# Optimization experiments

Hardware: AMD Instinct MI355X
Metric: run time of the kernel (lower is better)

## Reference

```python
import jax, jax.numpy as jnp
import numpy as np


def setup_inputs() -> dict:
    key = jax.random.key(0)
    kq, kk, kv = jax.random.split(key, 3)
    B, H, S, D = 2, 16, 2048, 128
    return {
        "q": jax.random.normal(kq, (B, H, S, D), dtype=jnp.float32),
        "k": jax.random.normal(kk, (B, H, S, D), dtype=jnp.float32),
        "v": jax.random.normal(kv, (B, H, S, D), dtype=jnp.float32),
    }


def reference(q, k, v):
    # scaled dot-product attention with causal mask (dropout in eval mode -> identity)
    d_k = k.shape[-1]
    scale = 1.0 / jnp.sqrt(jnp.asarray(d_k, dtype=q.dtype))
    # [B,H,Sq,Skv]
    attn = jnp.einsum("bhqd,bhkd->bhqk", q, k) * scale
    Sq = q.shape[-2]
    causal = jnp.triu(jnp.ones((Sq, Sq), dtype=bool), k=1)  # True above diagonal -> masked
    attn = jnp.where(causal, -jnp.inf, attn)
    attn = jax.nn.softmax(attn, axis=-1)
    return jnp.einsum("bhqk,bhkd->bhqd", attn, v)
```

## Files before the change

### kernel.cpp

```cpp
#include <hip/hip_runtime.h>

#define SQ 2048
#define DH 128
#define KVB 64
#define BHN 32
#define ELEMS ((size_t)BHN * SQ * DH)

typedef __bf16 bf16x8 __attribute__((ext_vector_type(8)));
typedef float f32x16 __attribute__((ext_vector_type(16)));

__device__ __forceinline__ f32x16 mfma32(bf16x8 a, bf16x8 b, f32x16 c){
  return __builtin_amdgcn_mfma_f32_32x32x16_bf16(a, b, c, 0, 0, 0);
}

#define EXP2 __builtin_amdgcn_exp2f

__device__ __forceinline__ unsigned short f2bf(float f){
  unsigned u = __builtin_bit_cast(unsigned, f);
  u += 0x7fffu + ((u >> 16) & 1u);
  return (unsigned short)(u >> 16);
}
__device__ __forceinline__ unsigned packbf(float a, float b){
  return (unsigned)f2bf(a) | ((unsigned)f2bf(b) << 16);
}

__device__ __forceinline__ void swap32(unsigned a, unsigned b, bool h, unsigned &x, unsigned &y){
  unsigned sb = __shfl_xor(b, 32);
  unsigned sa = __shfl_xor(a, 32);
  x = h ? sb : a;
  y = h ? b : sa;
}

__device__ __forceinline__ bf16x8 mkfrag(unsigned w0, unsigned w1, unsigned w2, unsigned w3){
  uint4 t; t.x = w0; t.y = w1; t.z = w2; t.w = w3;
  return __builtin_bit_cast(bf16x8, t);
}

__global__ __launch_bounds__(256, 4)
void convkv(const float* __restrict__ K, const float* __restrict__ V,
            unsigned short* __restrict__ Kb, unsigned short* __restrict__ Vb){
  const size_t g = (size_t)blockIdx.x * 256 + threadIdx.x;
  #pragma unroll
  for (int i = 0; i < 4; ++i){
    size_t e = (g + (size_t)i * 262144) * 8;
    float4 a = *(const float4*)(K + e);
    float4 b = *(const float4*)(K + e + 4);
    uint4 o;
    o.x = packbf(a.x, a.y); o.y = packbf(a.z, a.w);
    o.z = packbf(b.x, b.y); o.w = packbf(b.z, b.w);
    *(uint4*)(Kb + e) = o;
    a = *(const float4*)(V + e);
    b = *(const float4*)(V + e + 4);
    o.x = packbf(a.x, a.y); o.y = packbf(a.z, a.w);
    o.z = packbf(b.x, b.y); o.w = packbf(b.z, b.w);
    *(uint4*)(Vb + e) = o;
  }
}

template<bool BF16IN>
__global__ __launch_bounds__(512, 2)
void attn_fwd(const float* __restrict__ Q,
              const float* __restrict__ Kf,
              const float* __restrict__ Vf,
              const unsigned short* __restrict__ Kbg,
              const unsigned short* __restrict__ Vbg,
              float* __restrict__ O)
{
  __shared__ __align__(16) unsigned char smem[65536];
  float* SF = (float*)smem;

  const int tid  = threadIdx.x;
  const int lane = tid & 63;
  const int wid  = tid >> 6;
  const int rg   = wid & 3;
  const int par  = wid >> 2;
  const int col  = lane & 31;
  const int hi   = lane >> 5;
  const int i4   = lane & 3;
  const int d0   = (lane >> 2)*8;

  const int b   = blockIdx.x;
  const int xcd = b & 7;
  const int seq = b >> 3;
  const int bh4 = seq & 3;
  const int j   = seq >> 2;
  const int bh  = xcd + 8*bh4;

  const size_t base = (size_t)bh * SQ * DH;
  const float* Qg = Q + base;
  const float* Kg = Kf + base;
  const float* Vg = Vf + base;
  const unsigned short* Kgb = Kbg + base;
  const unsigned short* Vgb = Vbg + base;
  float* Og = O + base;

  const float SC = 0.08838834764831845f * 1.4426950408889634f;

  float4 kr[4], vr[4];
  uint4  krb[2], vrb[2];

  auto LOADT = [&](int kvb){
    if constexpr (BF16IN){
      #pragma unroll
      for (int i = 0; i < 2; ++i){
        int c = i*512 + tid, r = c >> 4, dc = c & 15;
        krb[i] = *(const uint4*)(Kgb + (size_t)(kvb + r)*DH + dc*8);
      }
      #pragma unroll
      for (int it = 0; it < 2; ++it){
        int row = wid*8 + it*4 + i4;
        vrb[it] = *(const uint4*)(Vgb + (size_t)(kvb + row)*DH + d0);
      }
    } else {
      #pragma unroll
      for (int i = 0; i < 2; ++i){
        int c = i*512 + tid, r = c >> 4, dc = c & 15;
        const float* src = Kg + (size_t)(kvb + r)*DH + dc*8;
        kr[2*i]   = *(const float4*)(src);
        kr[2*i+1] = *(const float4*)(src + 4);
      }
      #pragma unroll
      for (int it = 0; it < 2; ++it){
        int row = wid*8 + it*4 + i4;
        const float* src = Vg + (size_t)(kvb + row)*DH + d0;
        vr[2*it]   = *(const float4*)(src);
        vr[2*it+1] = *(const float4*)(src + 4);
      }
    }
  };

  auto STORET = [&](int bsel){
    const int bb = bsel * 32768;
    #pragma unroll
    for (int i = 0; i < 2; ++i){
      int c = i*512 + tid, r = c >> 4, dc = c & 15;
      uint4 kv;
      if constexpr (BF16IN){
        kv = krb[i];
      } else {
        kv.x = packbf(kr[2*i].x,   kr[2*i].y);
        kv.y = packbf(kr[2*i].z,   kr[2*i].w);
        kv.z = packbf(kr[2*i+1].x, kr[2*i+1].y);
        kv.w = packbf(kr[2*i+1].z, kr[2*i+1].w);
      }
      *(uint4*)&smem[bb + r*256 + ((dc*16) ^ ((r & 7) << 4))] = kv;
    }
    #pragma unroll
    for (int it = 0; it < 2; ++it){
      int r0 = wid*8 + it*4;
      unsigned M0, M1, M2, M3;
      if constexpr (BF16IN){
        M0 = vrb[it].x; M1 = vrb[it].y; M2 = vrb[it].z; M3 = vrb[it].w;
      } else {
        M0 = packbf(vr[2*it].x,   vr[2*it].y);
        M1 = packbf(vr[2*it].z,   vr[2*it].w);
        M2 = packbf(vr[2*it+1].x, vr[2*it+1].y);
        M3 = packbf(vr[2*it+1].z, vr[2*it+1].w);
      }
      unsigned t0=__shfl_xor(M1,1), t1=__shfl_xor(M0,1), t2=__shfl_xor(M3,1), t3=__shfl_xor(M2,1);
      bool ob1 = i4 & 1;
      unsigned N0 = ob1 ? t0 : M0;
      unsigned N1 = ob1 ? M1 : t1;
      unsigned N2 = ob1 ? t2 : M2;
      unsigned N3 = ob1 ? M3 : t3;
      unsigned u0s=__shfl_xor(N2,2), u1s=__shfl_xor(N3,2), u2s=__shfl_xor(N0,2), u3s=__shfl_xor(N1,2);
      bool ob2 = i4 & 2;
      unsigned F0 = ob2 ? u0s : N0;
      unsigned F1 = ob2 ? u1s : N1;
      unsigned F2 = ob2 ? N2 : u2s;
      unsigned F3 = ob2 ? N3 : u3s;
      int d = d0 + 2*i4;
      unsigned lo0 = (F0 & 0xffffu) | (F1 << 16);
      unsigned lo1 = (F2 & 0xffffu) | (F3 << 16);
      unsigned hi0 = (F0 >> 16) | (F1 & 0xffff0000u);
      unsigned hi1 = (F2 >> 16) | (F3 & 0xffff0000u);
      int cb = r0*2;
      int sA = ((d >> 1) & 7) << 4;
      *(uint2*)&smem[bb + 16384 + d*128     + (cb ^ sA)] = make_uint2(lo0, lo1);
      *(uint2*)&smem[bb + 16384 + (d+1)*128 + (cb ^ sA)] = make_uint2(hi0, hi1);
    }
  };

  #pragma unroll 1
  for (int ph = 0; ph < 2; ++ph){
    const int qt = ph ? j : (15 - j);
    const int nt = 2*qt + 2;
    const int Q0 = qt*128 + rg*32;
    const int qg = Q0 + col;

    bf16x8 qf[8];
    #pragma unroll
    for (int dc = 0; dc < 8; ++dc){
      const float* src = Qg + (size_t)qg*DH + dc*16 + hi*8;
      float4 f0 = *(const float4*)(src);
      float4 f1 = *(const float4*)(src + 4);
      uint4 tq;
      tq.x = packbf(f0.x, f0.y); tq.y = packbf(f0.z, f0.w);
      tq.z = packbf(f1.x, f1.y); tq.w = packbf(f1.z, f1.w);
      qf[dc] = __builtin_bit_cast(bf16x8, tq);
    }

    f32x16 o0 = {}, o1 = {}, o2 = {}, o3 = {};
    float m = -1e30f, lsum = 0.f;

    LOADT(0);
    STORET(0);
    __syncthreads();

    #pragma unroll 1
    for (int t = 0; t < nt; ++t){
      const int kvb = t * KVB;
      const int bb  = (t & 1) * 32768;
      const int myk = kvb + par*32;

      if (t + 1 < nt) LOADT(kvb + KVB);

      if (myk <= Q0 + 31){
        f32x16 s0 = {};
        const int krow = par*32 + col;
        #pragma unroll
        for (int dc = 0; dc < 8; ++dc){
          uint4 rk = *(const uint4*)&smem[bb + krow*256 + ((dc*32 + hi*16) ^ ((krow & 7) << 4))];
          s0 = mfma32(__builtin_bit_cast(bf16x8, rk), qf[dc], s0);
        }

        s0 = s0 * SC;
        if (myk + 31 > Q0){
          #pragma unroll
          for (int r = 0; r < 16; ++r){
            int kl = (r & 3) + 8*(r >> 2) + 4*hi;
            if (myk + kl > qg) s0[r] = -1e30f;
          }
        }

        float tmax = -1e30f;
        #pragma unroll
        for (int r = 0; r < 16; ++r) tmax = fmaxf(tmax, s0[r]);
        tmax = fmaxf(tmax, __shfl_xor(tmax, 32));
        if (!__all(tmax <= m + 8.0f)){
          float mnew  = fmaxf(m, tmax);
          float alpha = EXP2(m - mnew);
          m = mnew;
          lsum *= alpha;
          o0 *= alpha; o1 *= alpha; o2 *= alpha; o3 *= alpha;
        }

        float ps = 0.f;
        #pragma unroll
        for (int r = 0; r < 16; ++r){ float e = EXP2(s0[r] - m); s0[r] = e; ps += e; }
        lsum += ps;

        unsigned ua0 = packbf(s0[0],  s0[1]),  ua1 = packbf(s0[2],  s0[3]);
        unsigned ua2 = packbf(s0[4],  s0[5]),  ua3 = packbf(s0[6],  s0[7]);
        unsigned ua4 = packbf(s0[8],  s0[9]),  ua5 = packbf(s0[10], s0[11]);
        unsigned ua6 = packbf(s0[12], s0[13]), ua7 = packbf(s0[14], s0[15]);
        bool h = (bool)hi;
        unsigned w0, w1, w2, w3;
        bf16x8 pf[2];
        swap32(ua0, ua2, h, w0, w2); swap32(ua1, ua3, h, w1, w3); pf[0] = mkfrag(w0,w1,w2,w3);
        swap32(ua4, ua6, h, w0, w2); swap32(ua5, ua7, h, w1, w3); pf[1] = mkfrag(w0,w1,w2,w3);

        #pragma unroll
        for (int cc = 0; cc < 2; ++cc){
          #pragma unroll
          for (int db = 0; db < 4; ++db){
            int rowd = db*32 + col;
            uint4 rv = *(const uint4*)&smem[bb + 16384 + rowd*128 + ((par*64 + cc*32 + hi*16) ^ (((rowd >> 1) & 7) << 4))];
            f32x16& oo = (db==0)?o0:(db==1)?o1:(db==2)?o2:o3;
            oo = mfma32(__builtin_bit_cast(bf16x8, rv), pf[cc], oo);
          }
        }
      }

      if (t + 1 < nt) STORET((t + 1) & 1);
      __syncthreads();
    }

    lsum += __shfl_xor(lsum, 32);

    float a0 = 1.f, a1 = 0.f, inv = 0.f;
    #pragma unroll 1
    for (int round = 0; round < 2; ++round){
      const f32x16& pa = round ? o2 : o0;
      const f32x16& pb = round ? o3 : o1;
      if (par == 1){
        #pragma unroll
        for (int i = 0; i < 16; ++i){
          SF[rg*2048 + i*64 + lane]      = pa[i];
          SF[rg*2048 + (16+i)*64 + lane] = pb[i];
        }
        if (round == 0){
          SF[8192 + rg*64 + lane] = m;
          SF[8448 + rg*64 + lane] = lsum;
        }
      }
      __syncthreads();
      if (par == 0){
        if (round == 0){
          float m1 = SF[8192 + rg*64 + lane];
          float l1 = SF[8448 + rg*64 + lane];
          float ms = fmaxf(m, m1);
          a0 = EXP2(m - ms);
          a1 = EXP2(m1 - ms);
          float ls = lsum*a0 + l1*a1;
          inv = 1.0f / ls;
        }
        #pragma unroll
        for (int dbi = 0; dbi < 2; ++dbi){
          const f32x16& oo = round ? (dbi ? o3 : o2) : (dbi ? o1 : o0);
          const int db = round*2 + dbi;
          #pragma unroll
          for (int rg2 = 0; rg2 < 4; ++rg2){
            float4 w;
            w.x = (oo[rg2*4+0]*a0 + SF[rg*2048 + (dbi*16 + rg2*4+0)*64 + lane]*a1) * inv;
            w.y = (oo[rg2*4+1]*a0 + SF[rg*2048 + (dbi*16 + rg2*4+1)*64 + lane]*a1) * inv;
            w.z = (oo[rg2*4+2]*a0 + SF[rg*2048 + (dbi*16 + rg2*4+2)*64 + lane]*a1) * inv;
            w.w = (oo[rg2*4+3]*a0 + SF[rg*2048 + (dbi*16 + rg2*4+3)*64 + lane]*a1) * inv;
            *(float4*)(Og + (size_t)qg*DH + db*32 + rg2*8 + hi*4) = w;
          }
        }
      }
      __syncthreads();
    }
  }
}

extern "C" void kernel_launch(void* const* d_in, const int* in_sizes, int n_in,
                              void* d_out, int out_size, void* d_ws, size_t ws_size,
                              hipStream_t stream) {
  const float* q = (const float*)d_in[0];
  const float* k = (const float*)d_in[1];
  const float* v = (const float*)d_in[2];
  float* out = (float*)d_out;

  const size_t need = 2 * ELEMS * sizeof(unsigned short);
  if (ws_size >= need){
    unsigned short* kb = (unsigned short*)d_ws;
    unsigned short* vb = kb + ELEMS;
    convkv<<<1024, 256, 0, stream>>>(k, v, kb, vb);
    attn_fwd<true><<<256, 512, 0, stream>>>(q, k, v, kb, vb, out);
  } else {
    attn_fwd<false><<<256, 512, 0, stream>>>(q, k, v, nullptr, nullptr, out);
  }
}
```

Before: 96.29 us.

## Split paired causal q-tiles into separate blocks and add MFMA priority hints

Each block used to handle two query tiles in sequence (a long one and a short one, to balance causal work). Now each tile gets its own block, doubling the grid to 512 blocks, and the hardware scheduler does the balancing instead. Around the two MFMA loops, s_setprio is raised so matrix work is favoured over the other waves' loads. The trade-off is losing the guaranteed per-block balance and paying Q loading and setup per tile, in exchange for more concurrency and occupancy across CUs.

```diff
diff --git a/kernel.cpp b/kernel.cpp
--- a/kernel.cpp
+++ b/kernel.cpp
@@ -79,12 +79,16 @@
   const int i4   = lane & 3;
   const int d0   = (lane >> 2)*8;
 
-  const int b   = blockIdx.x;
-  const int xcd = b & 7;
-  const int seq = b >> 3;
-  const int bh4 = seq & 3;
-  const int j   = seq >> 2;
-  const int bh  = xcd + 8*bh4;
+  const int b    = blockIdx.x;
+  const int half = b >> 8;
+  const int bb8  = b & 255;
+  const int xcd  = bb8 & 7;
+  const int i    = bb8 >> 3;
+  const int bh4  = i & 3;
+  const int j    = i >> 2;
+  const int bh   = xcd + 8*bh4;
+  const int qt   = half ? j : (15 - j);
+  const int nt   = 2*qt + 2;
 
   const size_t base = (size_t)bh * SQ * DH;
   const float* Qg = Q + base;
@@ -102,9 +106,9 @@
   auto LOADT = [&](int kvb){
     if constexpr (BF16IN){
       #pragma unroll
-      for (int i = 0; i < 2; ++i){
-        int c = i*512 + tid, r = c >> 4, dc = c & 15;
-        krb[i] = *(const uint4*)(Kgb + (size_t)(kvb + r)*DH + dc*8);
+      for (int i2 = 0; i2 < 2; ++i2){
+        int c = i2*512 + tid, r = c >> 4, dc = c & 15;
+        krb[i2] = *(const uint4*)(Kgb + (size_t)(kvb + r)*DH + dc*8);
       }
       #pragma unroll
       for (int it = 0; it < 2; ++it){
@@ -113,11 +117,11 @@
       }
     } else {
       #pragma unroll
-      for (int i = 0; i < 2; ++i){
-        int c = i*512 + tid, r = c >> 4, dc = c & 15;
+      for (int i2 = 0; i2 < 2; ++i2){
+        int c = i2*512 + tid, r = c >> 4, dc = c & 15;
         const float* src = Kg + (size_t)(kvb + r)*DH + dc*8;
-        kr[2*i]   = *(const float4*)(src);
-        kr[2*i+1] = *(const float4*)(src + 4);
+        kr[2*i2]   = *(const float4*)(src);
+        kr[2*i2+1] = *(const float4*)(src + 4);
       }
       #pragma unroll
       for (int it = 0; it < 2; ++it){
@@ -130,20 +134,20 @@
   };
 
   auto STORET = [&](int bsel){
-    const int bb = bsel * 32768;
+    const int bboff = bsel * 32768;
     #pragma unroll
-    for (int i = 0; i < 2; ++i){
-      int c = i*512 + tid, r = c >> 4, dc = c & 15;
+    for (int i2 = 0; i2 < 2; ++i2){
+      int c = i2*512 + tid, r = c >> 4, dc = c & 15;
       uint4 kv;
       if constexpr (BF16IN){
-        kv = krb[i];
+        kv = krb[i2];
       } else {
-        kv.x = packbf(kr[2*i].x,   kr[2*i].y);
-        kv.y = packbf(kr[2*i].z,   kr[2*i].w);
-        kv.z = packbf(kr[2*i+1].x, kr[2*i+1].y);
-        kv.w = packbf(kr[2*i+1].z, kr[2*i+1].w);
-      }
-      *(uint4*)&smem[bb + r*256 + ((dc*16) ^ ((r & 7) << 4))] = kv;
+        kv.x = packbf(kr[2*i2].x,   kr[2*i2].y);
+        kv.y = packbf(kr[2*i2].z,   kr[2*i2].w);
+        kv.z = packbf(kr[2*i2+1].x, kr[2*i2+1].y);
+        kv.w = packbf(kr[2*i2+1].z, kr[2*i2+1].w);
+      }
+      *(uint4*)&smem[bboff + r*256 + ((dc*16) ^ ((r & 7) << 4))] = kv;
     }
     #pragma unroll
     for (int it = 0; it < 2; ++it){
@@ -176,152 +180,151 @@
       unsigned hi1 = (F2 >> 16) | (F3 & 0xffff0000u);
       int cb = r0*2;
       int sA = ((d >> 1) & 7) << 4;
-      *(uint2*)&smem[bb + 16384 + d*128     + (cb ^ sA)] = make_uint2(lo0, lo1);
-      *(uint2*)&smem[bb + 16384 + (d+1)*128 + (cb ^ sA)] = make_uint2(hi0, hi1);
+      *(uint2*)&smem[bboff + 16384 + d*128     + (cb ^ sA)] = make_uint2(lo0, lo1);
+      *(uint2*)&smem[bboff + 16384 + (d+1)*128 + (cb ^ sA)] = make_uint2(hi0, hi1);
     }
   };
 
+  const int Q0 = qt*128 + rg*32;
+  const int qg = Q0 + col;
+
+  bf16x8 qf[8];
+  #pragma unroll
+  for (int dc = 0; dc < 8; ++dc){
+    const float* src = Qg + (size_t)qg*DH + dc*16 + hi*8;
+    float4 f0 = *(const float4*)(src);
+    float4 f1 = *(const float4*)(src + 4);
+    uint4 tq;
+    tq.x = packbf(f0.x, f0.y); tq.y = packbf(f0.z, f0.w);
+    tq.z = packbf(f1.x, f1.y); tq.w = packbf(f1.z, f1.w);
+    qf[dc] = __builtin_bit_cast(bf16x8, tq);
+  }
+
+  f32x16 o0 = {}, o1 = {}, o2 = {}, o3 = {};
+  float m = -1e30f, lsum = 0.f;
+
+  LOADT(0);
+  STORET(0);
+  __syncthreads();
+
   #pragma unroll 1
-  for (int ph = 0; ph < 2; ++ph){
-    const int qt = ph ? j : (15 - j);
-    const int nt = 2*qt + 2;
-    const int Q0 = qt*128 + rg*32;
-    const int qg = Q0 + col;
-
-    bf16x8 qf[8];
-    #pragma unroll
-    for (int dc = 0; dc < 8; ++dc){
-      const float* src = Qg + (size_t)qg*DH + dc*16 + hi*8;
-      float4 f0 = *(const float4*)(src);
-      float4 f1 = *(const float4*)(src + 4);
-      uint4 tq;
-      tq.x = packbf(f0.x, f0.y); tq.y = packbf(f0.z, f0.w);
-      tq.z = packbf(f1.x, f1.y); tq.w = packbf(f1.z, f1.w);
-      qf[dc] = __builtin_bit_cast(bf16x8, tq);
-    }
-
-    f32x16 o0 = {}, o1 = {}, o2 = {}, o3 = {};
-    float m = -1e30f, lsum = 0.f;
-
-    LOADT(0);
-    STORET(0);
+  for (int t = 0; t < nt; ++t){
+    const int kvb = t * KVB;
+    const int bboff = (t & 1) * 32768;
+    const int myk = kvb + par*32;
+
+    if (t + 1 < nt) LOADT(kvb + KVB);
+
+    if (myk <= Q0 + 31){
+      f32x16 s0 = {};
+      const int krow = par*32 + col;
+      __builtin_amdgcn_s_setprio(1);
+      #pragma unroll
+      for (int dc = 0; dc < 8; ++dc){
+        uint4 rk = *(const uint4*)&smem[bboff + krow*256 + ((dc*32 + hi*16) ^ ((krow & 7) << 4))];
+        s0 = mfma32(__builtin_bit_cast(bf16x8, rk), qf[dc], s0);
+      }
+      __builtin_amdgcn_s_setprio(0);
+
+      s0 = s0 * SC;
+      if (myk + 31 > Q0){
+        #pragma unroll
+        for (int r = 0; r < 16; ++r){
+          int kl = (r & 3) + 8*(r >> 2) + 4*hi;
+          if (myk + kl > qg) s0[r] = -1e30f;
+        }
+      }
+
+      float tmax = -1e30f;
+      #pragma unroll
+      for (int r = 0; r < 16; ++r) tmax = fmaxf(tmax, s0[r]);
+      tmax = fmaxf(tmax, __shfl_xor(tmax, 32));
+      if (!__all(tmax <= m + 8.0f)){
+        float mnew  = fmaxf(m, tmax);
+        float alpha = EXP2(m - mnew);
+        m = mnew;
+        lsum *= alpha;
+        o0 *= alpha; o1 *= alpha; o2 *= alpha; o3 *= alpha;
+      }
+
+      float ps = 0.f;
+      #pragma unroll
+      for (int r = 0; r < 16; ++r){ float e = EXP2(s0[r] - m); s0[r] = e; ps += e; }
+      lsum += ps;
+
+      unsigned ua0 = packbf(s0[0],  s0[1]),  ua1 = packbf(s0[2],  s0[3]);
+      unsigned ua2 = packbf(s0[4],  s0[5]),  ua3 = packbf(s0[6],  s0[7]);
+      unsigned ua4 = packbf(s0[8],  s0[9]),  ua5 = packbf(s0[10], s0[11]);
+      unsigned ua6 = packbf(s0[12], s0[13]), ua7 = packbf(s0[14], s0[15]);
+      bool h = (bool)hi;
+      unsigned w0, w1, w2, w3;
+      bf16x8 pf[2];
+      swap32(ua0, ua2, h, w0, w2); swap32(ua1, ua3, h, w1, w3); pf[0] = mkfrag(w0,w1,w2,w3);
+      swap32(ua4, ua6, h, w0, w2); swap32(ua5, ua7, h, w1, w3); pf[1] = mkfrag(w0,w1,w2,w3);
+
+      __builtin_amdgcn_s_setprio(1);
+      #pragma unroll
+      for (int cc = 0; cc < 2; ++cc){
+        #pragma unroll
+        for (int db = 0; db < 4; ++db){
+          int rowd = db*32 + col;
+          uint4 rv = *(const uint4*)&smem[bboff + 16384 + rowd*128 + ((par*64 + cc*32 + hi*16) ^ (((rowd >> 1) & 7) << 4))];
+          f32x16& oo = (db==0)?o0:(db==1)?o1:(db==2)?o2:o3;
+          oo = mfma32(__builtin_bit_cast(bf16x8, rv), pf[cc], oo);
+        }
+      }
+      __builtin_amdgcn_s_setprio(0);
+    }
+
+    if (t + 1 < nt) STORET((t + 1) & 1);
     __syncthreads();
-
-    #pragma unroll 1
-    for (int t = 0; t < nt; ++t){
-      const int kvb = t * KVB;
-      const int bb  = (t & 1) * 32768;
-      const int myk = kvb + par*32;
-
-      if (t + 1 < nt) LOADT(kvb + KVB);
-
-      if (myk <= Q0 + 31){
-        f32x16 s0 = {};
-        const int krow = par*32 + col;
+  }
+
+  lsum += __shfl_xor(lsum, 32);
+
+  float a0 = 1.f, a1 = 0.f, inv = 0.f;
+  #pragma unroll 1
+  for (int round = 0; round < 2; ++round){
+    const f32x16& pa = round ? o2 : o0;
+    const f32x16& pb = round ? o3 : o1;
+    if (par == 1){
+      #pragma unroll
+      for (int i2 = 0; i2 < 16; ++i2){
+        SF[rg*2048 + i2*64 + lane]      = pa[i2];
+        SF[rg*2048 + (16+i2)*64 + lane] = pb[i2];
+      }
+      if (round == 0){
+        SF[8192 + rg*64 + lane] = m;
+        SF[8448 + rg*64 + lane] = lsum;
+      }
+    }
+    __syncthreads();
+    if (par == 0){
+      if (round == 0){
+        float m1 = SF[8192 + rg*64 + lane];
+        float l1 = SF[8448 + rg*64 + lane];
+        float ms = fmaxf(m, m1);
+        a0 = EXP2(m - ms);
+        a1 = EXP2(m1 - ms);
+        float ls = lsum*a0 + l1*a1;
+        inv = 1.0f / ls;
+      }
+      #pragma unroll
+      for (int dbi = 0; dbi < 2; ++dbi){
+        const f32x16& oo = round ? (dbi ? o3 : o2) : (dbi ? o1 : o0);
+        const int db = round*2 + dbi;
         #pragma unroll
-        for (int dc = 0; dc < 8; ++dc){
-          uint4 rk = *(const uint4*)&smem[bb + krow*256 + ((dc*32 + hi*16) ^ ((krow & 7) << 4))];
-          s0 = mfma32(__builtin_bit_cast(bf16x8, rk), qf[dc], s0);
+        for (int rg2 = 0; rg2 < 4; ++rg2){
+          float4 w;
+          w.x = (oo[rg2*4+0]*a0 + SF[rg*2048 + (dbi*16 + rg2*4+0)*64 + lane]*a1) * inv;
+          w.y = (oo[rg2*4+1]*a0 + SF[rg*2048 + (dbi*16 + rg2*4+1)*64 + lane]*a1) * inv;
+          w.z = (oo[rg2*4+2]*a0 + SF[rg*2048 + (dbi*16 + rg2*4+2)*64 + lane]*a1) * inv;
+          w.w = (oo[rg2*4+3]*a0 + SF[rg*2048 + (dbi*16 + rg2*4+3)*64 + lane]*a1) * inv;
+          *(float4*)(Og + (size_t)qg*DH + db*32 + rg2*8 + hi*4) = w;
         }
-
-        s0 = s0 * SC;
-        if (myk + 31 > Q0){
-          #pragma unroll
-          for (int r = 0; r < 16; ++r){
-            int kl = (r & 3) + 8*(r >> 2) + 4*hi;
-            if (myk + kl > qg) s0[r] = -1e30f;
-          }
-        }
-
-        float tmax = -1e30f;
-        #pragma unroll
-        for (int r = 0; r < 16; ++r) tmax = fmaxf(tmax, s0[r]);
-        tmax = fmaxf(tmax, __shfl_xor(tmax, 32));
-        if (!__all(tmax <= m + 8.0f)){
-          float mnew  = fmaxf(m, tmax);
-          float alpha = EXP2(m - mnew);
-          m = mnew;
-          lsum *= alpha;
-          o0 *= alpha; o1 *= alpha; o2 *= alpha; o3 *= alpha;
-        }
-
-        float ps = 0.f;
-        #pragma unroll
-        for (int r = 0; r < 16; ++r){ float e = EXP2(s0[r] - m); s0[r] = e; ps += e; }
-        lsum += ps;
-
-        unsigned ua0 = packbf(s0[0],  s0[1]),  ua1 = packbf(s0[2],  s0[3]);
-        unsigned ua2 = packbf(s0[4],  s0[5]),  ua3 = packbf(s0[6],  s0[7]);
-        unsigned ua4 = packbf(s0[8],  s0[9]),  ua5 = packbf(s0[10], s0[11]);
-        unsigned ua6 = packbf(s0[12], s0[13]), ua7 = packbf(s0[14], s0[15]);
-        bool h = (bool)hi;
-        unsigned w0, w1, w2, w3;
-        bf16x8 pf[2];
-        swap32(ua0, ua2, h, w0, w2); swap32(ua1, ua3, h, w1, w3); pf[0] = mkfrag(w0,w1,w2,w3);
-        swap32(ua4, ua6, h, w0, w2); swap32(ua5, ua7, h, w1, w3); pf[1] = mkfrag(w0,w1,w2,w3);
-
-        #pragma unroll
-        for (int cc = 0; cc < 2; ++cc){
-          #pragma unroll
-          for (int db = 0; db < 4; ++db){
-            int rowd = db*32 + col;
-            uint4 rv = *(const uint4*)&smem[bb + 16384 + rowd*128 + ((par*64 + cc*32 + hi*16) ^ (((rowd >> 1) & 7) << 4))];
-            f32x16& oo = (db==0)?o0:(db==1)?o1:(db==2)?o2:o3;
-            oo = mfma32(__builtin_bit_cast(bf16x8, rv), pf[cc], oo);
-          }
-        }
-      }
-
-      if (t + 1 < nt) STORET((t + 1) & 1);
-      __syncthreads();
-    }
-
-    lsum += __shfl_xor(lsum, 32);
-
-    float a0 = 1.f, a1 = 0.f, inv = 0.f;
-    #pragma unroll 1
-    for (int round = 0; round < 2; ++round){
-      const f32x16& pa = round ? o2 : o0;
-      const f32x16& pb = round ? o3 : o1;
-      if (par == 1){
-        #pragma unroll
-        for (int i = 0; i < 16; ++i){
-          SF[rg*2048 + i*64 + lane]      = pa[i];
-          SF[rg*2048 + (16+i)*64 + lane] = pb[i];
-        }
-        if (round == 0){
-          SF[8192 + rg*64 + lane] = m;
-          SF[8448 + rg*64 + lane] = lsum;
-        }
-      }
-      __syncthreads();
-      if (par == 0){
-        if (round == 0){
-          float m1 = SF[8192 + rg*64 + lane];
-          float l1 = SF[8448 + rg*64 + lane];
-          float ms = fmaxf(m, m1);
-          a0 = EXP2(m - ms);
-          a1 = EXP2(m1 - ms);
-          float ls = lsum*a0 + l1*a1;
-          inv = 1.0f / ls;
-        }
-        #pragma unroll
-        for (int dbi = 0; dbi < 2; ++dbi){
-          const f32x16& oo = round ? (dbi ? o3 : o2) : (dbi ? o1 : o0);
-          const int db = round*2 + dbi;
-          #pragma unroll
-          for (int rg2 = 0; rg2 < 4; ++rg2){
-            float4 w;
-            w.x = (oo[rg2*4+0]*a0 + SF[rg*2048 + (dbi*16 + rg2*4+0)*64 + lane]*a1) * inv;
-            w.y = (oo[rg2*4+1]*a0 + SF[rg*2048 + (dbi*16 + rg2*4+1)*64 + lane]*a1) * inv;
-            w.z = (oo[rg2*4+2]*a0 + SF[rg*2048 + (dbi*16 + rg2*4+2)*64 + lane]*a1) * inv;
-            w.w = (oo[rg2*4+3]*a0 + SF[rg*2048 + (dbi*16 + rg2*4+3)*64 + lane]*a1) * inv;
-            *(float4*)(Og + (size_t)qg*DH + db*32 + rg2*8 + hi*4) = w;
-          }
-        }
-      }
-      __syncthreads();
-    }
+      }
+    }
+    __syncthreads();
   }
 }
 
@@ -338,8 +341,8 @@
     unsigned short* kb = (unsigned short*)d_ws;
     unsigned short* vb = kb + ELEMS;
     convkv<<<1024, 256, 0, stream>>>(k, v, kb, vb);
-    attn_fwd<true><<<256, 512, 0, stream>>>(q, k, v, kb, vb, out);
+    attn_fwd<true><<<512, 512, 0, stream>>>(q, k, v, kb, vb, out);
   } else {
-    attn_fwd<false><<<256, 512, 0, stream>>>(q, k, v, nullptr, nullptr, out);
-  }
-}
+    attn_fwd<false><<<512, 512, 0, stream>>>(q, k, v, nullptr, nullptr, out);
+  }
+}
```

New measurement: 111.8 us. 16.1% more time.
